# Optimization experiments

Hardware: AMD Instinct MI355X
Metric: run time of the kernel (lower is better)

## Reference

```python
import jax, jax.numpy as jnp
import numpy as np

DIM, DFF, NH = 768, 2048, 12
HD = DIM // NH
N, NOBJ, L = 16, 52, 24
EPS = 1e-5


def setup_inputs() -> dict:
    key = jax.random.key(0)
    ks = jax.random.split(key, 16)
    g = lambda k, shape: jax.random.normal(k, shape, jnp.float32) * 0.02
    inp = {
        "lang": jax.random.normal(ks[0], (N, L, DIM), jnp.float32),
        "obj": jax.random.normal(ks[1], (N, NOBJ, DIM), jnp.float32),
        "lang_mask": jnp.ones((N, L), jnp.int32),
        "obj_mask": jnp.ones((N, NOBJ), jnp.int32),
        "co_mask": jnp.ones((N, L, NOBJ), jnp.int32),
    }
    # two multi-head attention blocks (edge / node): q,k,v,o projections
    for i, nm in enumerate(["e_wq", "e_wk", "e_wv", "e_wo", "n_wq", "n_wk", "n_wv", "n_wo"]):
        inp[nm] = g(ks[2 + i], (DIM, DIM))
        inp[nm.replace("w", "b")] = jnp.zeros((DIM,), jnp.float32)
    inp["ffn_w1"] = g(ks[10], (2 * DIM, DFF)); inp["ffn_b1"] = jnp.zeros((DFF,), jnp.float32)
    inp["ffn_w2"] = g(ks[11], (DFF, DIM)); inp["ffn_b2"] = jnp.zeros((DIM,), jnp.float32)
    for nm in ["ln_e", "ln_q", "ln2"]:
        inp[nm + "_g"] = jnp.ones((DIM,), jnp.float32)
        inp[nm + "_b"] = jnp.zeros((DIM,), jnp.float32)
    return inp


def _layernorm(x, g, b):
    m = jnp.mean(x, -1, keepdims=True)
    v = jnp.mean((x - m) ** 2, -1, keepdims=True)
    return (x - m) * jax.lax.rsqrt(v + EPS) * g + b


def _fwd(lang, obj, co_mask,
         e_wq, e_bq, e_wk, e_bk, e_wv, e_bv, e_wo, e_bo,
         n_wq, n_bq, n_wk, n_bk, n_wv, n_bv, n_wo, n_bo,
         ffn_w1, ffn_b1, ffn_w2, ffn_b2,
         ln_e_g, ln_e_b, ln_q_g, ln_q_b, ln2_g, ln2_b):
    scale = jnp.float32(1.0 / np.sqrt(HD))
    co_t = co_mask.swapaxes(1, 2)  # [N, nobj, L]: query objects attend over lang keys

    # ---- node branch: standard cross-attention obj -> lang ----
    qh = (obj @ n_wq + n_bq).reshape(N, NOBJ, NH, HD)
    kh = (lang @ n_wk + n_bk).reshape(N, L, NH, HD)
    vh = (lang @ n_wv + n_bv).reshape(N, L, NH, HD)
    s = jnp.einsum('nqhd,nlhd->nhql', qh, kh) * scale  # [N,H,nobj,L]
    s = jnp.where(co_t[:, None, :, :] > 0, s, jnp.float32(-1e9))
    a = jax.nn.softmax(s, axis=-1)
    node = jnp.einsum('nhql,nlhd->nqhd', a, vh).reshape(N, NOBJ, DIM) @ n_wo + n_bo

    # ---- edge branch: pairwise diffs attend over lang, then max over partner ----
    diff = obj[:, :, None, :] - obj[:, None, :, :]            # [N,i,j,D]
    qhe = (diff @ e_wq + e_bq).reshape(N, NOBJ, NOBJ, NH, HD)
    khe = (lang @ e_wk + e_bk).reshape(N, L, NH, HD)
    vhe = (lang @ e_wv + e_bv).reshape(N, L, NH, HD)
    se = jnp.einsum('nijhd,nlhd->nhijl', qhe, khe) * scale    # [N,H,i,j,L]
    # mask depends on (n, j, l): torch repeats co_mask^T over the i batch dim
    se = jnp.where(co_t[:, None, None, :, :] > 0, se, jnp.float32(-1e9))
    ae = jax.nn.softmax(se, axis=-1)
    oe = jnp.einsum('nhijl,nlhd->nijhd', ae, vhe).reshape(N, NOBJ, NOBJ, DIM)
    oe = oe @ e_wo + e_bo                                      # [N,i,j,D]
    edge = jnp.max(oe, axis=2)                                 # max over query/partner j -> [N,i,D]

    # ---- fuse ----
    xe = _layernorm(obj + edge, ln_e_g, ln_e_b)
    xn = _layernorm(obj + node, ln_q_g, ln_q_b)
    h = jnp.concatenate((xn, xe), -1)
    h = jax.nn.relu(h @ ffn_w1 + ffn_b1) @ ffn_w2 + ffn_b2
    return _layernorm(xn + h, ln2_g, ln2_b)


def reference(lang, obj, lang_mask, obj_mask, co_mask,
              e_wq, e_bq, e_wk, e_bk, e_wv, e_bv, e_wo, e_bo,
              n_wq, n_bq, n_wk, n_bk, n_wv, n_bv, n_wo, n_bo,
              ffn_w1, ffn_b1, ffn_w2, ffn_b2,
              ln_e_g, ln_e_b, ln_q_g, ln_q_b, ln2_g, ln2_b):
    return _fwd(lang, obj, co_mask,
                e_wq, e_bq, e_wk, e_bk, e_wv, e_bv, e_wo, e_bo,
                n_wq, n_bq, n_wk, n_bk, n_wv, n_bv, n_wo, n_bo,
                ffn_w1, ffn_b1, ffn_w2, ffn_b2,
                ln_e_g, ln_e_b, ln_q_g, ln_q_b, ln2_g, ln2_b)
```

## Files before the change

### kernel.cpp

```cpp
#include <hip/hip_runtime.h>
#include <math.h>

#define NOBJ 52
#define LL 24
#define NHEAD 12

typedef __attribute__((ext_vector_type(8))) short bf16x8;
typedef __attribute__((ext_vector_type(4))) float f32x4;
typedef __attribute__((ext_vector_type(4))) unsigned int u32x4;
typedef __attribute__((ext_vector_type(2))) unsigned int u32x2;

__device__ __forceinline__ unsigned short f2b(float x) {
    union { float f; unsigned int u; } v; v.f = x;
    unsigned int r = v.u + 0x7fffu + ((v.u >> 16) & 1u);
    return (unsigned short)(r >> 16);
}
__device__ __forceinline__ float b2f(unsigned short u) {
    union { unsigned int u; float f; } v; v.u = ((unsigned int)u) << 16;
    return v.f;
}
__device__ __forceinline__ unsigned int pack2(float a, float b) {
    return (unsigned int)f2b(a) | ((unsigned int)f2b(b) << 16);
}
__device__ __forceinline__ f32x4 mfma16(bf16x8 a, bf16x8 b, f32x4 c) {
    return __builtin_amdgcn_mfma_f32_16x16x32_bf16(a, b, c, 0, 0, 0);
}
__device__ __forceinline__ void gl_lds16(const void* g, void* lds) {
    __builtin_amdgcn_global_load_lds(
        (const __attribute__((address_space(1))) unsigned int*)g,
        (__attribute__((address_space(3))) unsigned int*)lds, 16, 0, 0);
}

__device__ __forceinline__ void transpose_tile(const float* __restrict__ src,
    unsigned short* __restrict__ dst, int K, int N, int t, char* smem)
{
    float (*ts)[65] = (float(*)[65])smem;
    const int tid = threadIdx.x;
    const int ntk = K >> 6;
    const int k0 = (t % ntk) << 6, n0 = (t / ntk) << 6;
    const int tx = tid & 63, ty = tid >> 6;
    #pragma unroll
    for (int i2 = 0; i2 < 16; ++i2) {
        const int row = i2 * 4 + ty;
        ts[row][tx] = src[(size_t)(k0 + row) * N + n0 + tx];
    }
    __syncthreads();
    #pragma unroll
    for (int i2 = 0; i2 < 16; ++i2) {
        const int row = i2 * 4 + ty;
        dst[(size_t)(n0 + row) * K + k0 + tx] = f2b(ts[tx][row]);
    }
}

__global__ __launch_bounds__(256)
void pack1_kernel(const float* s0, const float* s1, const float* s2,
                  const float* s3, const float* s4, const float* s5,
                  const float* s6, const float* s7,
                  unsigned short* d0, unsigned short* d1, unsigned short* d2,
                  unsigned short* d3, unsigned short* d4, unsigned short* d5,
                  unsigned short* d6, unsigned short* d7,
                  const float* obj, const float* lang, const float* n_bq,
                  const float* e_bk, const float* e_bv,
                  const float* n_bk, const float* n_bv,
                  unsigned short* objb, unsigned short* langb,
                  float* bqc, float* blc)
{
    __shared__ __align__(16) char smem[16640];
    const int bid = blockIdx.x;
    const int tid = threadIdx.x;
    if (bid < 1152) {
        const int job = bid / 144, t = bid % 144;
        const float* src; unsigned short* dst;
        switch (job) {
            case 0: src = s0; dst = d0; break;
            case 1: src = s1; dst = d1; break;
            case 2: src = s2; dst = d2; break;
            case 3: src = s3; dst = d3; break;
            case 4: src = s4; dst = d4; break;
            case 5: src = s5; dst = d5; break;
            case 6: src = s6; dst = d6; break;
            default: src = s7; dst = d7; break;
        }
        transpose_tile(src, dst, 768, 768, t, smem);
    } else {
        const int base = ((bid - 1152) * 256 + tid) * 4;
        const int T0 = 638976, T1 = 933888, T2 = 935424, T3 = 938496;
        if (base >= T3) return;
        if (base < T0) {
            f32x4 v = *(const f32x4*)(obj + base);
            *(u32x2*)(objb + base) = (u32x2){pack2(v[0], v[1]), pack2(v[2], v[3])};
        } else if (base < T1) {
            const int j = base - T0;
            f32x4 v = *(const f32x4*)(lang + j);
            *(u32x2*)(langb + j) = (u32x2){pack2(v[0], v[1]), pack2(v[2], v[3])};
        } else if (base < T2) {
            const int j = base - T1;
            if (j < 768) { *(f32x4*)(bqc + j) = (f32x4){0.f, 0.f, 0.f, 0.f}; }
            else         { *(f32x4*)(bqc + j) = *(const f32x4*)(n_bq + j - 768); }
        } else {
            const int j = base - T2;
            const int s = j / 768, c = j % 768;
            const float* p = (s == 0) ? e_bk : (s == 1) ? e_bv : (s == 2) ? n_bk : n_bv;
            *(f32x4*)(blc + j) = *(const f32x4*)(p + c);
        }
    }
}

struct GemmJob {
    const unsigned short* A; const unsigned short* Bt; const float* bias;
    float* C; unsigned short* Cb;
    int lda, ldb, ldc, K, nbx, nb, relu, swz;
};

__device__ __forceinline__ void gemm_body(const GemmJob J, int bid, char* smem)
{
    unsigned short* As = (unsigned short*)smem;
    unsigned short* Bs = (unsigned short*)(smem + 16384);
    int bx, by;
    if (J.swz) {
        const int cpx = J.nb >> 3;
        const int gid = (bid & 7) * cpx + (bid >> 3);
        const int nbm = J.nb / J.nbx;
        bx = gid / nbm; by = gid % nbm;
    } else { bx = bid % J.nbx; by = bid / J.nbx; }
    const int n0 = bx * 128, m0 = by * 64;
    const int tid = threadIdx.x;
    const int lane = tid & 63;
    const int w = tid >> 6, wr = w >> 1, wc = w & 1;
    const int lr = lane & 15, lk = lane >> 4;
    const int lda = J.lda, ldb = J.ldb, K = J.K;
    const unsigned short* Ab = J.A + (size_t)m0 * lda;
    const unsigned short* Bb = J.Bt + (size_t)n0 * ldb;

    f32x4 acc[2][4] = {};
    const int NT = K >> 6;

    #pragma unroll
    for (int q = 0; q < 2; ++q) {
        const int c = q * 256 + tid, row = c >> 3, p = (c & 7) ^ (row & 7);
        gl_lds16(Ab + (size_t)row * lda + p * 8, As + c * 8);
    }
    #pragma unroll
    for (int q = 0; q < 4; ++q) {
        const int c = q * 256 + tid, row = c >> 3, p = (c & 7) ^ (row & 7);
        gl_lds16(Bb + (size_t)row * ldb + p * 8, Bs + c * 8);
    }
    __syncthreads();

    for (int t = 0; t < NT; ++t) {
        const int cur = t & 1;
        if (t + 1 < NT) {
            const int k0 = (t + 1) << 6;
            #pragma unroll
            for (int q = 0; q < 2; ++q) {
                const int c = q * 256 + tid, row = c >> 3, p = (c & 7) ^ (row & 7);
                gl_lds16(Ab + (size_t)row * lda + k0 + p * 8, As + (cur ^ 1) * 4096 + c * 8);
            }
            #pragma unroll
            for (int q = 0; q < 4; ++q) {
                const int c = q * 256 + tid, row = c >> 3, p = (c & 7) ^ (row & 7);
                gl_lds16(Bb + (size_t)row * ldb + k0 + p * 8, Bs + (cur ^ 1) * 8192 + c * 8);
            }
        }
        #pragma unroll
        for (int kk = 0; kk < 2; ++kk) {
            bf16x8 af[2], bv[4];
            #pragma unroll
            for (int mt = 0; mt < 2; ++mt) {
                const int row = wr * 32 + mt * 16 + lr;
                const int pc = (kk * 4 + lk) ^ (row & 7);
                af[mt] = *(const bf16x8*)(As + cur * 4096 + row * 64 + pc * 8);
            }
            #pragma unroll
            for (int nt = 0; nt < 4; ++nt) {
                const int col = wc * 64 + nt * 16 + lr;
                const int pc = (kk * 4 + lk) ^ (col & 7);
                bv[nt] = *(const bf16x8*)(Bs + cur * 8192 + col * 64 + pc * 8);
            }
            #pragma unroll
            for (int mt = 0; mt < 2; ++mt)
                #pragma unroll
                for (int nt = 0; nt < 4; ++nt)
                    acc[mt][nt] = mfma16(af[mt], bv[nt], acc[mt][nt]);
        }
        __syncthreads();
    }

    #pragma unroll
    for (int mt = 0; mt < 2; ++mt) {
        #pragma unroll
        for (int nt = 0; nt < 4; ++nt) {
            const int col = n0 + wc * 64 + nt * 16 + lr;
            const float bvv = J.bias ? J.bias[col] : 0.f;
            #pragma unroll
            for (int r = 0; r < 4; ++r) {
                const int row = m0 + wr * 32 + mt * 16 + lk * 4 + r;
                float v = acc[mt][nt][r] + bvv;
                if (J.relu) v = fmaxf(v, 0.f);
                if (J.C)  J.C[(size_t)row * J.ldc + col] = v;
                if (J.Cb) J.Cb[(size_t)row * J.ldc + col] = f2b(v);
            }
        }
    }
}

__global__ __launch_bounds__(256)
void gemm_tn4(GemmJob j0, GemmJob j1, GemmJob j2, GemmJob j3)
{
    __shared__ __align__(16) char smem[49152];
    int bid = blockIdx.x;
    if (bid < j0.nb) { gemm_body(j0, bid, smem); return; }
    bid -= j0.nb;
    if (bid < j1.nb) { gemm_body(j1, bid, smem); return; }
    bid -= j1.nb;
    if (bid < j2.nb) { gemm_body(j2, bid, smem); return; }
    bid -= j2.nb;
    gemm_body(j3, bid, smem);
}

__global__ __launch_bounds__(256)
void proj_pack_kernel(GemmJob j0, GemmJob j1,
                      const float* w1, const float* w2,
                      unsigned short* W1t, unsigned short* W2t)
{
    __shared__ __align__(16) char smem[49152];
    int bid = blockIdx.x;
    if (bid < j0.nb) { gemm_body(j0, bid, smem); return; }
    bid -= j0.nb;
    if (bid < j1.nb) { gemm_body(j1, bid, smem); return; }
    const int t = bid - j1.nb;
    if (t < 768) transpose_tile(w1, W1t, 1536, 2048, t, smem);
    else transpose_tile(w2, W2t, 2048, 768, t - 768, smem);
}

__global__ __launch_bounds__(256)
void mid3_kernel(const unsigned short* __restrict__ QCb,
                 const unsigned short* __restrict__ LCb,
                 const unsigned short* __restrict__ Wet,
                 const unsigned short* __restrict__ Wot,
                 const float* __restrict__ e_bq,
                 unsigned short* __restrict__ VWe,
                 unsigned short* __restrict__ VWn,
                 float* __restrict__ S2e, float* __restrict__ Tb,
                 float* __restrict__ S2n)
{
    __shared__ __align__(16) union USm {
        struct { unsigned short As[8192], Bs[8192]; } g;
        unsigned short Ct[128 * 136];
        struct { float sA[52][68], sB[24][68]; } s;
    } U;
    const int bid = blockIdx.x;
    const int tid = threadIdx.x;

    if (bid < 432) {
        const int sub = bid >= 216;
        const int b = sub ? bid - 216 : bid;
        const int aoff = sub ? 2304 : 768;
        const unsigned short* Bt = sub ? Wot : Wet;
        unsigned short* Vout = sub ? VWn : VWe;

        const int h = b / 18, rm = b % 18, mt = rm / 6, ntile = rm % 6;
        const int m0 = mt * 128, n0 = ntile * 128;
        const int lane = tid & 63, w = tid >> 6, wr = w >> 1, wc = w & 1;
        const int lr = lane & 15, lk = lane >> 4;
        #pragma unroll
        for (int q = 0; q < 4; ++q) {
            const int c = q * 256 + tid, row = c >> 3, p = (c & 7) ^ (row & 7);
            gl_lds16(LCb + (size_t)(m0 + row) * 3072 + aoff + h * 64 + p * 8, &U.g.As[c * 8]);
            gl_lds16(Bt + (size_t)(n0 + row) * 768 + h * 64 + p * 8, &U.g.Bs[c * 8]);
        }
        __syncthreads();
        f32x4 acc[4][4] = {};
        #pragma unroll
        for (int kk = 0; kk < 2; ++kk) {
            bf16x8 af[4], bv[4];
            #pragma unroll
            for (int m2 = 0; m2 < 4; ++m2) {
                const int row = wr * 64 + m2 * 16 + lr;
                const int pc = (kk * 4 + lk) ^ (row & 7);
                af[m2] = *(const bf16x8*)&U.g.As[row * 64 + pc * 8];
            }
            #pragma unroll
            for (int n2 = 0; n2 < 4; ++n2) {
                const int col = wc * 64 + n2 * 16 + lr;
                const int pc = (kk * 4 + lk) ^ (col & 7);
                bv[n2] = *(const bf16x8*)&U.g.Bs[col * 64 + pc * 8];
            }
            #pragma unroll
            for (int m2 = 0; m2 < 4; ++m2)
                #pragma unroll
                for (int n2 = 0; n2 < 4; ++n2)
                    acc[m2][n2] = mfma16(af[m2], bv[n2], acc[m2][n2]);
        }
        __syncthreads();
        #pragma unroll
        for (int m2 = 0; m2 < 4; ++m2)
            #pragma unroll
            for (int n2 = 0; n2 < 4; ++n2) {
                const int col = wc * 64 + n2 * 16 + lr;
                #pragma unroll
                for (int r = 0; r < 4; ++r) {
                    const int row = wr * 64 + m2 * 16 + lk * 4 + r;
                    U.Ct[row * 136 + col] = f2b(acc[m2][n2][r]);
                }
            }
        __syncthreads();
        #pragma unroll
        for (int q = 0; q < 8; ++q) {
            const int item = q * 256 + tid;
            const int dl = item & 127, kg = item >> 7;
            const int m = m0 + kg * 8;
            const int nn = m / 24, l0 = m % 24;
            const int kc = (h * 24 + l0) >> 3;
            const int ks = kc >> 2;
            const int dg = n0 + dl;
            const int kpos = (kc & 3) ^ ((dg >> 1) & 3);
            u32x4 uu;
            #pragma unroll
            for (int e = 0; e < 4; ++e)
                uu[e] = (unsigned int)U.Ct[(kg * 8 + 2 * e) * 136 + dl]
                      | ((unsigned int)U.Ct[(kg * 8 + 2 * e + 1) * 136 + dl] << 16);
            *(u32x4*)(Vout + (size_t)nn * 221184 + ks * 24576 + dg * 32 + kpos * 8) = uu;
        }
    } else {
        const int sub = bid >= 624;
        const int b = bid - (sub ? 624 : 432);
        const int n = b / NHEAD, h = b % NHEAD;
        const int qoff = sub ? 768 : 0, koff = sub ? 1536 : 0;
        float* Sout = sub ? S2n : S2e;
        for (int p = tid; p < 52 * 64; p += 256) {
            const int q = p >> 6, d = p & 63;
            U.s.sA[q][d] = b2f(QCb[(size_t)(n * 52 + q) * 1536 + qoff + h * 64 + d]);
        }
        for (int p = tid; p < 24 * 64; p += 256) {
            const int l = p >> 6, d = p & 63;
            U.s.sB[l][d] = b2f(LCb[(size_t)(n * 24 + l) * 3072 + koff + h * 64 + d]);
        }
        __syncthreads();
        for (int p = tid; p < 52 * 24; p += 256) {
            const int q = p / 24, l = p % 24;
            float s = 0.f;
            #pragma unroll
            for (int d = 0; d < 64; ++d) s += U.s.sA[q][d] * U.s.sB[l][d];
            Sout[((size_t)(n * NHEAD + h) * 52 + q) * 24 + l] = s;
        }
        if (!sub && tid < 24) {
            float s = 0.f;
            #pragma unroll
            for (int d = 0; d < 64; ++d) s += e_bq[h * 64 + d] * U.s.sB[tid][d];
            Tb[((size_t)n * NHEAD + h) * 24 + tid] = s;
        }
    }
}

__global__ __launch_bounds__(256)
void sm_kernel(const float* __restrict__ S2e, const float* __restrict__ Tb,
               const float* __restrict__ S2n, const int* __restrict__ co_mask,
               unsigned short* __restrict__ Pe, unsigned short* __restrict__ Pn)
{
    __shared__ __align__(16) unsigned short Ps[52 * 288];
    __shared__ float SiT[288];
    __shared__ unsigned char cmb[1248];
    const int bid = blockIdx.x;
    const int tid = threadIdx.x;

    if (bid < 832) {
        const int n = bid / 52, i = bid % 52;
        const float* S2x = S2e + (size_t)n * NHEAD * 52 * 24;
        for (int p = tid; p < 288; p += 256) {
            const int h = p / 24, l = p % 24;
            SiT[p] = S2x[((size_t)h * 52 + i) * 24 + l] + Tb[((size_t)n * NHEAD + h) * 24 + l];
        }
        for (int p = tid; p < 1248; p += 256)
            cmb[p] = (unsigned char)(co_mask[(size_t)n * 1248 + p] > 0);
        __syncthreads();
        for (int p = tid; p < 624; p += 256) {
            const int h = p / 52, j = p % 52;
            const float* Sj = S2x + ((size_t)h * 52 + j) * 24;
            const float* st = SiT + h * 24;
            float x[24]; float mx = -1e30f;
            #pragma unroll
            for (int l = 0; l < 24; ++l) {
                float v = (st[l] - Sj[l]) * 0.125f;
                v = cmb[l * 52 + j] ? v : -1e9f;
                x[l] = v; mx = fmaxf(mx, v);
            }
            float sum = 0.f;
            #pragma unroll
            for (int l = 0; l < 24; ++l) { const float e = __expf(x[l] - mx); x[l] = e; sum += e; }
            const float inv = 1.f / sum;
            u32x4* dst = (u32x4*)(Ps + j * 288 + h * 24);
            u32x4 u0, u1, u2;
            #pragma unroll
            for (int c = 0; c < 4; ++c) {
                u0[c] = pack2(x[2 * c] * inv, x[2 * c + 1] * inv);
                u1[c] = pack2(x[8 + 2 * c] * inv, x[9 + 2 * c] * inv);
                u2[c] = pack2(x[16 + 2 * c] * inv, x[17 + 2 * c] * inv);
            }
            dst[0] = u0; dst[1] = u1; dst[2] = u2;
        }
        __syncthreads();
        unsigned short* dstG = Pe + (size_t)bid * 14976;
        for (int p = tid; p < 1872; p += 256)
            *(u32x4*)(dstG + p * 8) = *(const u32x4*)(Ps + p * 8);
    } else {
        const int n = bid - 832;
        const float* S2x = S2n + (size_t)n * NHEAD * 52 * 24;
        for (int p = tid; p < 1248; p += 256)
            cmb[p] = (unsigned char)(co_mask[(size_t)n * 1248 + p] > 0);
        __syncthreads();
        for (int p = tid; p < 624; p += 256) {
            const int h = p / 52, q = p % 52;
            const float* Sq = S2x + ((size_t)h * 52 + q) * 24;
            float x[24]; float mx = -1e30f;
            #pragma unroll
            for (int l = 0; l < 24; ++l) {
                float v = Sq[l] * 0.125f;
                v = cmb[l * 52 + q] ? v : -1e9f;
                x[l] = v; mx = fmaxf(mx, v);
            }
            float sum = 0.f;
            #pragma unroll
            for (int l = 0; l < 24; ++l) { const float e = __expf(x[l] - mx); x[l] = e; sum += e; }
            const float inv = 1.f / sum;
            u32x4* dst = (u32x4*)(Ps + q * 288 + h * 24);
            u32x4 u0, u1, u2;
            #pragma unroll
            for (int c = 0; c < 4; ++c) {
                u0[c] = pack2(x[2 * c] * inv, x[2 * c + 1] * inv);
                u1[c] = pack2(x[8 + 2 * c] * inv, x[9 + 2 * c] * inv);
                u2[c] = pack2(x[16 + 2 * c] * inv, x[17 + 2 * c] * inv);
            }
            dst[0] = u0; dst[1] = u1; dst[2] = u2;
        }
        __syncthreads();
        unsigned short* dstG = Pn + (size_t)n * 14976;
        for (int p = tid; p < 1872; p += 256)
            *(u32x4*)(dstG + p * 8) = *(const u32x4*)(Ps + p * 8);
    }
}

__global__ __launch_bounds__(256)
void av_kernel(const unsigned short* __restrict__ Pe,
               const unsigned short* __restrict__ Pn,
               const unsigned short* __restrict__ VWe,
               const unsigned short* __restrict__ VWn,
               const float* __restrict__ ebo, const float* __restrict__ nbo,
               unsigned short* __restrict__ EdgeBb,
               unsigned short* __restrict__ NodePb)
{
    __shared__ __align__(16) char smem[40960];
    unsigned short* As = (unsigned short*)smem;
    unsigned short* Bs = (unsigned short*)(smem + 16384);
    const int bid = blockIdx.x;
    const int tid = threadIdx.x;
    const int lane = tid & 63, w = tid >> 6;
    const int lr = lane & 15, lk = lane >> 4;

    if (bid < 1664) {
        const int sw = (bid & 7) * 208 + (bid >> 3);
        const int n = sw / 104;
        const int r104 = sw % 104;
        const int ip = r104 >> 2, dq = r104 & 3;
        const int i0 = ip * 2;
        const unsigned short* Pa = Pe + (size_t)(n * 52 + i0) * 14976;
        const unsigned short* Bsrc = VWe + (size_t)n * 221184 + dq * 6144;

        const int ca0 = tid, ca1 = 256 + tid;
        const int ro0 = (ca0 >> 2) & 63, kp0 = ca0 & 3;
        const int ro1 = (ca1 >> 2) & 63, kp1 = ca1 & 3;
        const int sa0 = (ca0 >> 8) * 14976 + ro0 * 288 + ((kp0 ^ ((ro0 >> 1) & 3)) << 3);
        const int sa1 = (ca1 >> 8) * 14976 + ro1 * 288 + ((kp1 ^ ((ro1 >> 1) & 3)) << 3);

        gl_lds16(Pa + sa0, As + ca0 * 8);
        gl_lds16(Pa + sa1, As + ca1 * 8);
        #pragma unroll
        for (int q = 0; q < 3; ++q) {
            const int c = q * 256 + tid;
            gl_lds16(Bsrc + c * 8, Bs + c * 8);
        }
        __syncthreads();

        const int iw = w >> 1, cg = (w & 1) * 96;
        f32x4 acc[4][6] = {};
        for (int ks = 0; ks < 9; ++ks) {
            const int cur = ks & 1;
            if (ks < 8) {
                const int nb = cur ^ 1;
                gl_lds16(Pa + sa0 + (ks + 1) * 32, As + nb * 4096 + ca0 * 8);
                gl_lds16(Pa + sa1 + (ks + 1) * 32, As + nb * 4096 + ca1 * 8);
                #pragma unroll
                for (int q = 0; q < 3; ++q) {
                    const int c = q * 256 + tid;
                    gl_lds16(Bsrc + (size_t)(ks + 1) * 24576 + c * 8, Bs + nb * 6144 + c * 8);
                }
            }
            bf16x8 af[4];
            #pragma unroll
            for (int mt = 0; mt < 4; ++mt) {
                const int row = mt * 16 + lr;
                af[mt] = *(const bf16x8*)(As + cur * 4096 + iw * 2048 + row * 32
                                          + ((lk ^ ((row >> 1) & 3)) << 3));
            }
            #pragma unroll
            for (int nt = 0; nt < 6; ++nt) {
                const int cl = cg + nt * 16 + lr;
                bf16x8 bv = *(const bf16x8*)(Bs + cur * 6144 + cl * 32
                                             + ((lk ^ ((cl >> 1) & 3)) << 3));
                #pragma unroll
                for (int mt = 0; mt < 4; ++mt)
                    acc[mt][nt] = mfma16(af[mt], bv, acc[mt][nt]);
            }
            __syncthreads();
        }

        #pragma unroll
        for (int nt = 0; nt < 6; ++nt) {
            float m = -1e30f;
            #pragma unroll
            for (int mt = 0; mt < 4; ++mt)
                #pragma unroll
                for (int r = 0; r < 4; ++r) {
                    const int row = mt * 16 + lk * 4 + r;
                    if (row < NOBJ) m = fmaxf(m, acc[mt][nt][r]);
                }
            m = fmaxf(m, __shfl_xor(m, 16));
            m = fmaxf(m, __shfl_xor(m, 32));
            if (lk == 0) {
                const int col = dq * 192 + cg + nt * 16 + lr;
                EdgeBb[(size_t)(n * 52 + i0 + iw) * 768 + col] = f2b(m + ebo[col]);
            }
        }
    } else {
        const int t = bid - 1664;
        const int n = t >> 2, dq = t & 3;
        const unsigned short* Pa = Pn + (size_t)n * 14976;
        const unsigned short* Bsrc = VWn + (size_t)n * 221184 + dq * 6144;

        const int ro = (tid >> 2) & 63, kp = tid & 3;
        const int sa = ro * 288 + ((kp ^ ((ro >> 1) & 3)) << 3);

        gl_lds16(Pa + sa, As + tid * 8);
        #pragma unroll
        for (int q = 0; q < 3; ++q) {
            const int c = q * 256 + tid;
            gl_lds16(Bsrc + c * 8, Bs + c * 8);
        }
        __syncthreads();

        const int cg = w * 48;
        f32x4 acc[4][3] = {};
        for (int ks = 0; ks < 9; ++ks) {
            const int cur = ks & 1;
            if (ks < 8) {
                const int nb = cur ^ 1;
                gl_lds16(Pa + sa + (ks + 1) * 32, As + nb * 4096 + tid * 8);
                #pragma unroll
                for (int q = 0; q < 3; ++q) {
                    const int c = q * 256 + tid;
                    gl_lds16(Bsrc + (size_t)(ks + 1) * 24576 + c * 8, Bs + nb * 6144 + c * 8);
                }
            }
            bf16x8 af[4];
            #pragma unroll
            for (int mt = 0; mt < 4; ++mt) {
                const int row = mt * 16 + lr;
                af[mt] = *(const bf16x8*)(As + cur * 4096 + row * 32
                                          + ((lk ^ ((row >> 1) & 3)) << 3));
            }
            #pragma unroll
            for (int nt = 0; nt < 3; ++nt) {
                const int cl = cg + nt * 16 + lr;
                bf16x8 bv = *(const bf16x8*)(Bs + cur * 6144 + cl * 32
                                             + ((lk ^ ((cl >> 1) & 3)) << 3));
                #pragma unroll
                for (int mt = 0; mt < 4; ++mt)
                    acc[mt][nt] = mfma16(af[mt], bv, acc[mt][nt]);
            }
            __syncthreads();
        }

        #pragma unroll
        for (int nt = 0; nt < 3; ++nt) {
            const int col = dq * 192 + cg + nt * 16 + lr;
            const float bv = nbo[col];
            #pragma unroll
            for (int mt = 0; mt < 4; ++mt)
                #pragma unroll
                for (int r = 0; r < 4; ++r) {
                    const int row = mt * 16 + lk * 4 + r;
                    if (row < NOBJ)
                        NodePb[(size_t)(n * 52 + row) * 768 + col] = f2b(acc[mt][nt][r] + bv);
                }
        }
    }
}

__global__ __launch_bounds__(256)
void ln_dual_kernel(const float* __restrict__ obj,
                    const unsigned short* __restrict__ NodePb,
                    const unsigned short* __restrict__ EdgeBb,
                    const float* __restrict__ gq, const float* __restrict__ bq,
                    const float* __restrict__ ge, const float* __restrict__ be,
                    unsigned short* __restrict__ Fusedb)
{
    __shared__ float red[8];
    const int job = blockIdx.x >= 832;
    const int row = blockIdx.x - (job ? 832 : 0);
    const int tid = threadIdx.x;
    const unsigned short* x2 = (job ? EdgeBb : NodePb) + (size_t)row * 768;
    const float* x1 = obj + (size_t)row * 768;
    const float* g = job ? ge : gq;
    const float* bb = job ? be : bq;
    float v[3]; float s = 0.f;
    #pragma unroll
    for (int c = 0; c < 3; ++c) {
        const int col = tid + 256 * c;
        v[c] = x1[col] + b2f(x2[col]); s += v[c];
    }
    #pragma unroll
    for (int o = 32; o; o >>= 1) s += __shfl_xor(s, o);
    if ((tid & 63) == 0) red[tid >> 6] = s;
    __syncthreads();
    const float mean = (red[0] + red[1] + red[2] + red[3]) * (1.f / 768.f);
    float var = 0.f;
    #pragma unroll
    for (int c = 0; c < 3; ++c) { const float d = v[c] - mean; var += d * d; }
    #pragma unroll
    for (int o = 32; o; o >>= 1) var += __shfl_xor(var, o);
    __syncthreads();
    if ((tid & 63) == 0) red[4 + (tid >> 6)] = var;
    __syncthreads();
    const float vt = (red[4] + red[5] + red[6] + red[7]) * (1.f / 768.f);
    const float rs = rsqrtf(vt + 1e-5f);
    unsigned short* dst = Fusedb + (size_t)row * 1536 + (job ? 768 : 0);
    #pragma unroll
    for (int c = 0; c < 3; ++c) {
        const int col = tid + 256 * c;
        dst[col] = f2b((v[c] - mean) * rs * g[col] + bb[col]);
    }
}

__global__ __launch_bounds__(256)
void ln2_kernel(const unsigned short* __restrict__ x1b,
                const float* __restrict__ Hp, const float* __restrict__ b2,
                const float* __restrict__ g, const float* __restrict__ bb,
                float* __restrict__ dst)
{
    __shared__ float red[8];
    const int row = blockIdx.x, tid = threadIdx.x;
    float v[3]; float s = 0.f;
    #pragma unroll
    for (int c = 0; c < 3; ++c) {
        const int col = tid + 256 * c;
        const size_t o = (size_t)row * 768 + col;
        float h = Hp[o] + Hp[638976 + o] + Hp[2 * 638976 + o] + Hp[3 * 638976 + o];
        v[c] = b2f(x1b[(size_t)row * 1536 + col]) + h + b2[col];
        s += v[c];
    }
    #pragma unroll
    for (int o = 32; o; o >>= 1) s += __shfl_xor(s, o);
    if ((tid & 63) == 0) red[tid >> 6] = s;
    __syncthreads();
    const float mean = (red[0] + red[1] + red[2] + red[3]) * (1.f / 768.f);
    float var = 0.f;
    #pragma unroll
    for (int c = 0; c < 3; ++c) { const float d = v[c] - mean; var += d * d; }
    #pragma unroll
    for (int o = 32; o; o >>= 1) var += __shfl_xor(var, o);
    __syncthreads();
    if ((tid & 63) == 0) red[4 + (tid >> 6)] = var;
    __syncthreads();
    const float vt = (red[4] + red[5] + red[6] + red[7]) * (1.f / 768.f);
    const float rs = rsqrtf(vt + 1e-5f);
    #pragma unroll
    for (int c = 0; c < 3; ++c) {
        const int col = tid + 256 * c;
        dst[(size_t)row * 768 + col] = (v[c] - mean) * rs * g[col] + bb[col];
    }
}

extern "C" void kernel_launch(void* const* d_in, const int* in_sizes, int n_in,
                              void* d_out, int out_size, void* d_ws, size_t ws_size,
                              hipStream_t stream)
{
    (void)in_sizes; (void)n_in; (void)out_size; (void)ws_size;
    const float* lang  = (const float*)d_in[0];
    const float* obj   = (const float*)d_in[1];
    const int* co_mask = (const int*)d_in[4];
    const float* e_wq = (const float*)d_in[5];
    const float* e_bq = (const float*)d_in[6];
    const float* e_wk = (const float*)d_in[7];
    const float* e_bk = (const float*)d_in[8];
    const float* e_wv = (const float*)d_in[9];
    const float* e_bv = (const float*)d_in[10];
    const float* e_wo = (const float*)d_in[11];
    const float* e_bo = (const float*)d_in[12];
    const float* n_wq = (const float*)d_in[13];
    const float* n_bq = (const float*)d_in[14];
    const float* n_wk = (const float*)d_in[15];
    const float* n_bk = (const float*)d_in[16];
    const float* n_wv = (const float*)d_in[17];
    const float* n_bv = (const float*)d_in[18];
    const float* n_wo = (const float*)d_in[19];
    const float* n_bo = (const float*)d_in[20];
    const float* ffn_w1 = (const float*)d_in[21];
    const float* ffn_b1 = (const float*)d_in[22];
    const float* ffn_w2 = (const float*)d_in[23];
    const float* ffn_b2 = (const float*)d_in[24];
    const float* ln_e_g = (const float*)d_in[25];
    const float* ln_e_b = (const float*)d_in[26];
    const float* ln_q_g = (const float*)d_in[27];
    const float* ln_q_b = (const float*)d_in[28];
    const float* ln2_g = (const float*)d_in[29];
    const float* ln2_b = (const float*)d_in[30];
    float* out = (float*)d_out;

    char* wsb = (char*)d_ws;
    unsigned short* Wqt   = (unsigned short*)(wsb + 0);
    unsigned short* Wlt   = (unsigned short*)(wsb + 2359296);
    unsigned short* Wet   = (unsigned short*)(wsb + 7077888);
    unsigned short* Wot   = (unsigned short*)(wsb + 8257536);
    unsigned short* W1t   = (unsigned short*)(wsb + 9437184);
    unsigned short* W2t   = (unsigned short*)(wsb + 15728640);
    unsigned short* objb  = (unsigned short*)(wsb + 18874368);
    unsigned short* langb = (unsigned short*)(wsb + 20152320);
    float*          bqc   = (float*)(wsb + 20742144);
    float*          blc   = (float*)(wsb + 20748288);
    unsigned short* QCb   = (unsigned short*)(wsb + 20760576);
    unsigned short* LCb   = (unsigned short*)(wsb + 23316480);
    float*          S2e   = (float*)(wsb + 25675776);
    float*          Tb    = (float*)(wsb + 26634240);
    float*          S2n   = (float*)(wsb + 26652672);
    unsigned short* VWe   = (unsigned short*)(wsb + 27611136);
    unsigned short* VWn   = (unsigned short*)(wsb + 34689024);
    unsigned short* Pe    = (unsigned short*)(wsb + 41766912);
    unsigned short* Pn    = (unsigned short*)(wsb + 66686976);
    unsigned short* NodePb= (unsigned short*)(wsb + 67198976);
    unsigned short* EdgeBb= (unsigned short*)(wsb + 68476928);
    unsigned short* Fusedb= (unsigned short*)(wsb + 69754880);
    unsigned short* H1b   = (unsigned short*)(wsb + 72310784);
    float*          Hp    = (float*)(wsb + 75718656);

    dim3 blk(256);
    pack1_kernel<<<2069, blk, 0, stream>>>(
        e_wq, n_wq, e_wk, e_wv, n_wk, n_wv, n_wo, e_wo,
        Wqt, Wqt + 589824, Wlt, Wlt + 589824, Wlt + 2 * 589824, Wlt + 3 * 589824,
        Wot, Wet,
        obj, lang, n_bq, e_bk, e_bv, n_bk, n_bv, objb, langb, bqc, blc);
    {
        GemmJob p0 = {objb, Wqt, bqc, nullptr, QCb, 768, 768, 1536, 768, 12, 156, 0, 0};
        GemmJob p1 = {langb, Wlt, blc, nullptr, LCb, 768, 768, 3072, 768, 24, 144, 0, 0};
        proj_pack_kernel<<<1452, blk, 0, stream>>>(p0, p1, ffn_w1, ffn_w2, W1t, W2t);
    }
    mid3_kernel<<<816, blk, 0, stream>>>(QCb, LCb, Wet, Wot, e_bq,
                                         VWe, VWn, S2e, Tb, S2n);
    sm_kernel<<<848, blk, 0, stream>>>(S2e, Tb, S2n, co_mask, Pe, Pn);
    av_kernel<<<1728, blk, 0, stream>>>(Pe, Pn, VWe, VWn, e_bo, n_bo, EdgeBb, NodePb);
    ln_dual_kernel<<<1664, blk, 0, stream>>>(obj, NodePb, EdgeBb, ln_q_g, ln_q_b,
                                             ln_e_g, ln_e_b, Fusedb);
    {
        GemmJob p0 = {Fusedb, W1t, ffn_b1, nullptr, H1b, 1536, 1536, 2048, 1536, 16, 208, 1, 1};
        gemm_tn4<<<208, blk, 0, stream>>>(p0, p0, p0, p0);
    }
    {
        GemmJob q0 = {H1b,        W2t,        nullptr, Hp,               nullptr, 2048, 2048, 768, 512, 6, 78, 0, 0};
        GemmJob q1 = {H1b + 512,  W2t + 512,  nullptr, Hp + 638976,      nullptr, 2048, 2048, 768, 512, 6, 78, 0, 0};
        GemmJob q2 = {H1b + 1024, W2t + 1024, nullptr, Hp + 2 * 638976,  nullptr, 2048, 2048, 768, 512, 6, 78, 0, 0};
        GemmJob q3 = {H1b + 1536, W2t + 1536, nullptr, Hp + 3 * 638976,  nullptr, 2048, 2048, 768, 512, 6, 78, 0, 0};
        gemm_tn4<<<312, blk, 0, stream>>>(q0, q1, q2, q3);
    }
    ln2_kernel<<<832, blk, 0, stream>>>(Fusedb, Hp, ffn_b2, ln2_g, ln2_b, out);
}
```

Baseline: 125.2 us.

## Fuse softmax and attention-value GEMM into one kernel keeping probabilities in LDS

Merges the softmax kernel and the AV/output-projection kernel into a single 512-thread kernel. Each block computes the softmax probabilities for two query rows straight into a swizzled shared-memory tile and then runs the MFMA GEMM against streamed VW tiles. This removes the large bf16 probability tensors (Pe/Pn) round-tripping through global memory and one kernel launch. In exchange it uses about 124KB of LDS per block, which lowers occupancy, and each block now covers half the output columns instead of a quarter.

```diff
diff --git a/kernel.cpp b/kernel.cpp
--- a/kernel.cpp
+++ b/kernel.cpp
@@ -353,31 +353,56 @@
     }
 }
 
-__global__ __launch_bounds__(256)
-void sm_kernel(const float* __restrict__ S2e, const float* __restrict__ Tb,
-               const float* __restrict__ S2n, const int* __restrict__ co_mask,
-               unsigned short* __restrict__ Pe, unsigned short* __restrict__ Pn)
-{
-    __shared__ __align__(16) unsigned short Ps[52 * 288];
-    __shared__ float SiT[288];
-    __shared__ unsigned char cmb[1248];
+__global__ __launch_bounds__(512)
+void attn_kernel(const float* __restrict__ S2e, const float* __restrict__ Tb,
+                 const float* __restrict__ S2n, const int* __restrict__ co_mask,
+                 const unsigned short* __restrict__ VWe,
+                 const unsigned short* __restrict__ VWn,
+                 const float* __restrict__ ebo, const float* __restrict__ nbo,
+                 unsigned short* __restrict__ EdgeBb,
+                 unsigned short* __restrict__ NodePb)
+{
+    __shared__ __align__(16) char smem[126464];
+    unsigned short* Pf = (unsigned short*)smem;
+    unsigned short* Bs = (unsigned short*)(smem + 73728);
+    float* SiT = (float*)(smem + 122880);
+    unsigned char* cmb = (unsigned char*)(smem + 125184);
     const int bid = blockIdx.x;
     const int tid = threadIdx.x;
+    const int lane = tid & 63, w = tid >> 6;
+    const int lr = lane & 15, lk = lane >> 4;
 
     if (bid < 832) {
-        const int n = bid / 52, i = bid % 52;
+        const int sw = (bid & 7) * 104 + (bid >> 3);
+        const int n = sw / 52;
+        const int r52 = sw % 52;
+        const int ip = r52 >> 1, dh = r52 & 1;
+        const int i0 = ip * 2;
+        const unsigned short* Bsrc = VWe + (size_t)n * 221184 + dh * 12288;
         const float* S2x = S2e + (size_t)n * NHEAD * 52 * 24;
-        for (int p = tid; p < 288; p += 256) {
-            const int h = p / 24, l = p % 24;
-            SiT[p] = S2x[((size_t)h * 52 + i) * 24 + l] + Tb[((size_t)n * NHEAD + h) * 24 + l];
-        }
-        for (int p = tid; p < 1248; p += 256)
+
+        #pragma unroll
+        for (int q = 0; q < 3; ++q) {
+            const int c = q * 512 + tid;
+            gl_lds16(Bsrc + c * 8, Bs + c * 8);
+        }
+        for (int p = tid; p < 576; p += 512) {
+            const int ii = p >= 288 ? 1 : 0;
+            const int rl = p - ii * 288;
+            const int h = rl / 24, l = rl % 24;
+            SiT[ii * 288 + rl] = S2x[((size_t)h * 52 + i0 + ii) * 24 + l]
+                               + Tb[((size_t)n * NHEAD + h) * 24 + l];
+        }
+        for (int p = tid; p < 1248; p += 512)
             cmb[p] = (unsigned char)(co_mask[(size_t)n * 1248 + p] > 0);
         __syncthreads();
-        for (int p = tid; p < 624; p += 256) {
-            const int h = p / 52, j = p % 52;
+
+        for (int p = tid; p < 1248; p += 512) {
+            const int ii = p >= 624 ? 1 : 0;
+            const int rl = p - ii * 624;
+            const int h = rl / 52, j = rl % 52;
             const float* Sj = S2x + ((size_t)h * 52 + j) * 24;
-            const float* st = SiT + h * 24;
+            const float* st = SiT + ii * 288 + h * 24;
             float x[24]; float mx = -1e30f;
             #pragma unroll
             for (int l = 0; l < 24; ++l) {
@@ -389,123 +414,42 @@
             #pragma unroll
             for (int l = 0; l < 24; ++l) { const float e = __expf(x[l] - mx); x[l] = e; sum += e; }
             const float inv = 1.f / sum;
-            u32x4* dst = (u32x4*)(Ps + j * 288 + h * 24);
-            u32x4 u0, u1, u2;
-            #pragma unroll
-            for (int c = 0; c < 4; ++c) {
-                u0[c] = pack2(x[2 * c] * inv, x[2 * c + 1] * inv);
-                u1[c] = pack2(x[8 + 2 * c] * inv, x[9 + 2 * c] * inv);
-                u2[c] = pack2(x[16 + 2 * c] * inv, x[17 + 2 * c] * inv);
-            }
-            dst[0] = u0; dst[1] = u1; dst[2] = u2;
-        }
-        __syncthreads();
-        unsigned short* dstG = Pe + (size_t)bid * 14976;
-        for (int p = tid; p < 1872; p += 256)
-            *(u32x4*)(dstG + p * 8) = *(const u32x4*)(Ps + p * 8);
-    } else {
-        const int n = bid - 832;
-        const float* S2x = S2n + (size_t)n * NHEAD * 52 * 24;
-        for (int p = tid; p < 1248; p += 256)
-            cmb[p] = (unsigned char)(co_mask[(size_t)n * 1248 + p] > 0);
-        __syncthreads();
-        for (int p = tid; p < 624; p += 256) {
-            const int h = p / 52, q = p % 52;
-            const float* Sq = S2x + ((size_t)h * 52 + q) * 24;
-            float x[24]; float mx = -1e30f;
-            #pragma unroll
-            for (int l = 0; l < 24; ++l) {
-                float v = Sq[l] * 0.125f;
-                v = cmb[l * 52 + q] ? v : -1e9f;
-                x[l] = v; mx = fmaxf(mx, v);
-            }
-            float sum = 0.f;
-            #pragma unroll
-            for (int l = 0; l < 24; ++l) { const float e = __expf(x[l] - mx); x[l] = e; sum += e; }
-            const float inv = 1.f / sum;
-            u32x4* dst = (u32x4*)(Ps + q * 288 + h * 24);
-            u32x4 u0, u1, u2;
-            #pragma unroll
-            for (int c = 0; c < 4; ++c) {
-                u0[c] = pack2(x[2 * c] * inv, x[2 * c + 1] * inv);
-                u1[c] = pack2(x[8 + 2 * c] * inv, x[9 + 2 * c] * inv);
-                u2[c] = pack2(x[16 + 2 * c] * inv, x[17 + 2 * c] * inv);
-            }
-            dst[0] = u0; dst[1] = u1; dst[2] = u2;
-        }
-        __syncthreads();
-        unsigned short* dstG = Pn + (size_t)n * 14976;
-        for (int p = tid; p < 1872; p += 256)
-            *(u32x4*)(dstG + p * 8) = *(const u32x4*)(Ps + p * 8);
-    }
-}
-
-__global__ __launch_bounds__(256)
-void av_kernel(const unsigned short* __restrict__ Pe,
-               const unsigned short* __restrict__ Pn,
-               const unsigned short* __restrict__ VWe,
-               const unsigned short* __restrict__ VWn,
-               const float* __restrict__ ebo, const float* __restrict__ nbo,
-               unsigned short* __restrict__ EdgeBb,
-               unsigned short* __restrict__ NodePb)
-{
-    __shared__ __align__(16) char smem[40960];
-    unsigned short* As = (unsigned short*)smem;
-    unsigned short* Bs = (unsigned short*)(smem + 16384);
-    const int bid = blockIdx.x;
-    const int tid = threadIdx.x;
-    const int lane = tid & 63, w = tid >> 6;
-    const int lr = lane & 15, lk = lane >> 4;
-
-    if (bid < 1664) {
-        const int sw = (bid & 7) * 208 + (bid >> 3);
-        const int n = sw / 104;
-        const int r104 = sw % 104;
-        const int ip = r104 >> 2, dq = r104 & 3;
-        const int i0 = ip * 2;
-        const unsigned short* Pa = Pe + (size_t)(n * 52 + i0) * 14976;
-        const unsigned short* Bsrc = VWe + (size_t)n * 221184 + dq * 6144;
-
-        const int ca0 = tid, ca1 = 256 + tid;
-        const int ro0 = (ca0 >> 2) & 63, kp0 = ca0 & 3;
-        const int ro1 = (ca1 >> 2) & 63, kp1 = ca1 & 3;
-        const int sa0 = (ca0 >> 8) * 14976 + ro0 * 288 + ((kp0 ^ ((ro0 >> 1) & 3)) << 3);
-        const int sa1 = (ca1 >> 8) * 14976 + ro1 * 288 + ((kp1 ^ ((ro1 >> 1) & 3)) << 3);
-
-        gl_lds16(Pa + sa0, As + ca0 * 8);
-        gl_lds16(Pa + sa1, As + ca1 * 8);
-        #pragma unroll
-        for (int q = 0; q < 3; ++q) {
-            const int c = q * 256 + tid;
-            gl_lds16(Bsrc + c * 8, Bs + c * 8);
-        }
-        __syncthreads();
-
-        const int iw = w >> 1, cg = (w & 1) * 96;
+            unsigned short* Prow = Pf + ii * 18432 + j * 288;
+            const int swk = (j >> 1) & 3;
+            #pragma unroll
+            for (int c = 0; c < 3; ++c) {
+                u32x4 u;
+                #pragma unroll
+                for (int m = 0; m < 4; ++m)
+                    u[m] = pack2(x[c * 8 + 2 * m] * inv, x[c * 8 + 2 * m + 1] * inv);
+                *(u32x4*)(Prow + (((3 * h + c) ^ swk) << 3)) = u;
+            }
+        }
+        __syncthreads();
+
+        const int iw = w >> 2, cg = (w & 3) * 96;
         f32x4 acc[4][6] = {};
         for (int ks = 0; ks < 9; ++ks) {
             const int cur = ks & 1;
             if (ks < 8) {
-                const int nb = cur ^ 1;
-                gl_lds16(Pa + sa0 + (ks + 1) * 32, As + nb * 4096 + ca0 * 8);
-                gl_lds16(Pa + sa1 + (ks + 1) * 32, As + nb * 4096 + ca1 * 8);
+                const unsigned short* src = Bsrc + (size_t)(ks + 1) * 24576;
                 #pragma unroll
                 for (int q = 0; q < 3; ++q) {
-                    const int c = q * 256 + tid;
-                    gl_lds16(Bsrc + (size_t)(ks + 1) * 24576 + c * 8, Bs + nb * 6144 + c * 8);
+                    const int c = q * 512 + tid;
+                    gl_lds16(src + c * 8, Bs + (cur ^ 1) * 12288 + c * 8);
                 }
             }
             bf16x8 af[4];
             #pragma unroll
             for (int mt = 0; mt < 4; ++mt) {
                 const int row = mt * 16 + lr;
-                af[mt] = *(const bf16x8*)(As + cur * 4096 + iw * 2048 + row * 32
-                                          + ((lk ^ ((row >> 1) & 3)) << 3));
+                af[mt] = *(const bf16x8*)(Pf + iw * 18432 + row * 288
+                                          + (((ks * 4 + lk) ^ ((row >> 1) & 3)) << 3));
             }
             #pragma unroll
             for (int nt = 0; nt < 6; ++nt) {
                 const int cl = cg + nt * 16 + lr;
-                bf16x8 bv = *(const bf16x8*)(Bs + cur * 6144 + cl * 32
+                bf16x8 bv = *(const bf16x8*)(Bs + cur * 12288 + cl * 32
                                              + ((lk ^ ((cl >> 1) & 3)) << 3));
                 #pragma unroll
                 for (int mt = 0; mt < 4; ++mt)
@@ -527,24 +471,49 @@
             m = fmaxf(m, __shfl_xor(m, 16));
             m = fmaxf(m, __shfl_xor(m, 32));
             if (lk == 0) {
-                const int col = dq * 192 + cg + nt * 16 + lr;
+                const int col = dh * 384 + cg + nt * 16 + lr;
                 EdgeBb[(size_t)(n * 52 + i0 + iw) * 768 + col] = f2b(m + ebo[col]);
             }
         }
     } else {
-        const int t = bid - 1664;
-        const int n = t >> 2, dq = t & 3;
-        const unsigned short* Pa = Pn + (size_t)n * 14976;
-        const unsigned short* Bsrc = VWn + (size_t)n * 221184 + dq * 6144;
-
-        const int ro = (tid >> 2) & 63, kp = tid & 3;
-        const int sa = ro * 288 + ((kp ^ ((ro >> 1) & 3)) << 3);
-
-        gl_lds16(Pa + sa, As + tid * 8);
+        const int t = bid - 832;
+        const int n = t >> 1, dh = t & 1;
+        const unsigned short* Bsrc = VWn + (size_t)n * 221184 + dh * 12288;
+        const float* S2x = S2n + (size_t)n * NHEAD * 52 * 24;
+
         #pragma unroll
         for (int q = 0; q < 3; ++q) {
-            const int c = q * 256 + tid;
+            const int c = q * 512 + tid;
             gl_lds16(Bsrc + c * 8, Bs + c * 8);
+        }
+        for (int p = tid; p < 1248; p += 512)
+            cmb[p] = (unsigned char)(co_mask[(size_t)n * 1248 + p] > 0);
+        __syncthreads();
+
+        for (int p = tid; p < 624; p += 512) {
+            const int h = p / 52, q = p % 52;
+            const float* Sq = S2x + ((size_t)h * 52 + q) * 24;
+            float x[24]; float mx = -1e30f;
+            #pragma unroll
+            for (int l = 0; l < 24; ++l) {
+                float v = Sq[l] * 0.125f;
+                v = cmb[l * 52 + q] ? v : -1e9f;
+                x[l] = v; mx = fmaxf(mx, v);
+            }
+            float sum = 0.f;
+            #pragma unroll
+            for (int l = 0; l < 24; ++l) { const float e = __expf(x[l] - mx); x[l] = e; sum += e; }
+            const float inv = 1.f / sum;
+            unsigned short* Prow = Pf + q * 288;
+            const int swk = (q >> 1) & 3;
+            #pragma unroll
+            for (int c = 0; c < 3; ++c) {
+                u32x4 u;
+                #pragma unroll
+                for (int m = 0; m < 4; ++m)
+                    u[m] = pack2(x[c * 8 + 2 * m] * inv, x[c * 8 + 2 * m + 1] * inv);
+                *(u32x4*)(Prow + (((3 * h + c) ^ swk) << 3)) = u;
+            }
         }
         __syncthreads();
 
@@ -553,25 +522,24 @@
         for (int ks = 0; ks < 9; ++ks) {
             const int cur = ks & 1;
             if (ks < 8) {
-                const int nb = cur ^ 1;
-                gl_lds16(Pa + sa + (ks + 1) * 32, As + nb * 4096 + tid * 8);
+                const unsigned short* src = Bsrc + (size_t)(ks + 1) * 24576;
                 #pragma unroll
                 for (int q = 0; q < 3; ++q) {
-                    const int c = q * 256 + tid;
-                    gl_lds16(Bsrc + (size_t)(ks + 1) * 24576 + c * 8, Bs + nb * 6144 + c * 8);
+                    const int c = q * 512 + tid;
+                    gl_lds16(src + c * 8, Bs + (cur ^ 1) * 12288 + c * 8);
                 }
             }
             bf16x8 af[4];
             #pragma unroll
             for (int mt = 0; mt < 4; ++mt) {
                 const int row = mt * 16 + lr;
-                af[mt] = *(const bf16x8*)(As + cur * 4096 + row * 32
-                                          + ((lk ^ ((row >> 1) & 3)) << 3));
+                af[mt] = *(const bf16x8*)(Pf + row * 288
+                                          + (((ks * 4 + lk) ^ ((row >> 1) & 3)) << 3));
             }
             #pragma unroll
             for (int nt = 0; nt < 3; ++nt) {
                 const int cl = cg + nt * 16 + lr;
-                bf16x8 bv = *(const bf16x8*)(Bs + cur * 6144 + cl * 32
+                bf16x8 bv = *(const bf16x8*)(Bs + cur * 12288 + cl * 32
                                              + ((lk ^ ((cl >> 1) & 3)) << 3));
                 #pragma unroll
                 for (int mt = 0; mt < 4; ++mt)
@@ -582,7 +550,7 @@
 
         #pragma unroll
         for (int nt = 0; nt < 3; ++nt) {
-            const int col = dq * 192 + cg + nt * 16 + lr;
+            const int col = dh * 384 + cg + nt * 16 + lr;
             const float bv = nbo[col];
             #pragma unroll
             for (int mt = 0; mt < 4; ++mt)
@@ -734,13 +702,11 @@
     float*          S2n   = (float*)(wsb + 26652672);
     unsigned short* VWe   = (unsigned short*)(wsb + 27611136);
     unsigned short* VWn   = (unsigned short*)(wsb + 34689024);
-    unsigned short* Pe    = (unsigned short*)(wsb + 41766912);
-    unsigned short* Pn    = (unsigned short*)(wsb + 66686976);
-    unsigned short* NodePb= (unsigned short*)(wsb + 67198976);
-    unsigned short* EdgeBb= (unsigned short*)(wsb + 68476928);
-    unsigned short* Fusedb= (unsigned short*)(wsb + 69754880);
-    unsigned short* H1b   = (unsigned short*)(wsb + 72310784);
-    float*          Hp    = (float*)(wsb + 75718656);
+    unsigned short* NodePb= (unsigned short*)(wsb + 41766912);
+    unsigned short* EdgeBb= (unsigned short*)(wsb + 43044864);
+    unsigned short* Fusedb= (unsigned short*)(wsb + 44322816);
+    unsigned short* H1b   = (unsigned short*)(wsb + 46878720);
+    float*          Hp    = (float*)(wsb + 50286592);
 
     dim3 blk(256);
     pack1_kernel<<<2069, blk, 0, stream>>>(
@@ -755,8 +721,8 @@
     }
     mid3_kernel<<<816, blk, 0, stream>>>(QCb, LCb, Wet, Wot, e_bq,
                                          VWe, VWn, S2e, Tb, S2n);
-    sm_kernel<<<848, blk, 0, stream>>>(S2e, Tb, S2n, co_mask, Pe, Pn);
-    av_kernel<<<1728, blk, 0, stream>>>(Pe, Pn, VWe, VWn, e_bo, n_bo, EdgeBb, NodePb);
+    attn_kernel<<<864, dim3(512), 0, stream>>>(S2e, Tb, S2n, co_mask, VWe, VWn,
+                                               e_bo, n_bo, EdgeBb, NodePb);
     ln_dual_kernel<<<1664, blk, 0, stream>>>(obj, NodePb, EdgeBb, ln_q_g, ln_q_b,
                                              ln_e_g, ln_e_b, Fusedb);
     {
```

Measured after the change: 126.8 us. Within noise of the previous version (+1.3%).
